# Optimization experiments

Measured on AMD Instinct MI355X. Metric: run time of the kernel, lower is better.

Reference implementation:

```python
import jax, jax.numpy as jnp
import numpy as np

EPS = 1e-5

def _neighbor_idx(H, W):
    # flat index of the 3x3 clamped neighborhood for each pixel, [H*W, 9]
    r = np.arange(H)[:, None, None]  # [H,1,1]
    c = np.arange(W)[None, :, None]  # [1,W,1]
    dr = np.repeat(np.array([-1, 0, 1]), 3)[None, None, :]  # [1,1,9]
    dc = np.tile(np.array([-1, 0, 1]), 3)[None, None, :]
    ri = np.clip(r + dr, 0, H - 1)
    ci = np.clip(c + dc, 0, W - 1)
    return jnp.asarray((ri * W + ci).reshape(H * W, 9))

def setup_inputs() -> dict:
    key = jax.random.key(0)
    ks = jax.random.split(key, 7)
    B, C, H, W = 16, 256, 80, 80
    s = 1.0 / np.sqrt(C)
    return {
        "x": jax.random.normal(ks[0], (B, C, H, W), jnp.float32),
        "Wq": jax.random.normal(ks[1], (C, C), jnp.float32) * s,
        "bq": jax.random.normal(ks[2], (C,), jnp.float32) * s,
        "Wk": jax.random.normal(ks[3], (C, C), jnp.float32) * s,
        "bk": jax.random.normal(ks[4], (C,), jnp.float32) * s,
        "Wv": jax.random.normal(ks[5], (C, C), jnp.float32) * s,
        "bv": jax.random.normal(ks[6], (C,), jnp.float32) * s,
    }

def reference(x, Wq, bq, Wk, bk, Wv, bv):
    B, C, H, W = x.shape
    N = H * W
    xf = x.reshape(B, C, N)
    # 1x1 convs as channel GEMMs
    q = jnp.einsum('oc,bcn->bno', Wq, xf) + bq          # [B,N,C]
    k = jnp.einsum('oc,bcn->bon', Wk, xf) + bk[:, None]  # [B,C,N]
    v = jnp.einsum('oc,bcn->bon', Wv, xf) + bv[:, None]  # [B,C,N]
    idx = _neighbor_idx(H, W)                            # [N,9]
    k_n = k[:, :, idx]                                   # [B,C,N,9]
    v_n = v[:, :, idx]                                   # [B,C,N,9]
    # raw attention scores (NOT softmaxed before AV, matching the source)
    scores = jnp.einsum('bnc,bcnq->bnq', q, k_n)         # [B,N,9]
    new_v = jnp.einsum('bnq,bcnq->bcn', scores, v_n).reshape(B, C, H, W)
    out9 = scores.reshape(B, H, W, 9)
    center = out9[..., 4]
    others_mean = (out9.sum(-1) - center) / 8.0
    output = jnp.stack([center, others_mean], axis=-1)   # [B,H,W,2]
    # residual + layer_norm over [H,W] (no affine), per (B,C)
    xr = x + new_v
    mu = xr.mean(axis=(-2, -1), keepdims=True)
    var = ((xr - mu) ** 2).mean(axis=(-2, -1), keepdims=True)
    x_out = (xr - mu) * jax.lax.rsqrt(var + EPS)
    return (output, x_out)
```

## Files before the change

kernel.cpp:

```cpp
#include <hip/hip_runtime.h>
#include <hip/hip_bf16.h>

using f32x4  = __attribute__((ext_vector_type(4))) float;
using short8 = __attribute__((ext_vector_type(8))) short;
using bf16   = __hip_bfloat16;

constexpr int BATCH = 16;
constexpr int CH    = 256;
constexpr int HH    = 80;
constexpr int WW    = 80;
constexpr int NPIX  = HH * WW;

__device__ __forceinline__ float b2f(unsigned short u) {
    union { unsigned int i; float f; } x;
    x.i = ((unsigned int)u) << 16;
    return x.f;
}

typedef __attribute__((address_space(3))) void  lds_void;
typedef __attribute__((address_space(1))) const void glb_void;
__device__ __forceinline__ void glds16(const void* g, void* l) {
    __builtin_amdgcn_global_load_lds((glb_void*)(unsigned long long)g,
                                     (lds_void*)(unsigned int)(unsigned long long)l,
                                     16, 0, 0);
}

__global__ __launch_bounds__(256) void convert_w(
    const float* __restrict__ Wq, const float* __restrict__ Wk,
    const float* __restrict__ Wv, bf16* __restrict__ Wb)
{
    const int elem = blockIdx.x * 256 + threadIdx.x;
    const int mat  = blockIdx.y;
    const float* src = (mat == 0) ? Wq : (mat == 1) ? Wk : Wv;
    Wb[(size_t)mat * CH * CH + elem] = __float2bfloat16(src[elem]);
}

__global__ __launch_bounds__(256) void transpose_cast(
    const float* __restrict__ x, bf16* __restrict__ xt, int b0)
{
    __shared__ float t[64][65];
    const int b  = b0 + blockIdx.z;
    const int n0 = blockIdx.x * 64;
    const int c0 = blockIdx.y * 64;
    const float* xb = x + (size_t)b * CH * NPIX;
    const int tid = threadIdx.x;

    {
        const int nl  = tid & 63;
        const int cl0 = tid >> 6;
        #pragma unroll
        for (int i = 0; i < 16; ++i) {
            const int cl = cl0 + i * 4;
            t[cl][nl] = xb[(size_t)(c0 + cl) * NPIX + n0 + nl];
        }
    }
    __syncthreads();
    {
        bf16* xtb = xt + (size_t)blockIdx.z * NPIX * CH;
        const int cp  = (tid & 15) * 4;
        const int nl0 = tid >> 4;
        #pragma unroll
        for (int i = 0; i < 4; ++i) {
            const int nl = nl0 + i * 16;
            ushort4 pk;
            #pragma unroll
            for (int j = 0; j < 4; ++j) {
                const bf16 h = __float2bfloat16(t[cp + j][nl]);
                ((unsigned short*)&pk)[j] = *(const unsigned short*)&h;
            }
            *(ushort4*)(xtb + (size_t)(n0 + nl) * CH + c0 + cp) = pk;
        }
    }
}

__global__ __launch_bounds__(256, 2) void qkv_mfma(
    const bf16* __restrict__ xt, const bf16* __restrict__ Wb,
    const float* __restrict__ bq, const float* __restrict__ bk,
    const float* __restrict__ bv,
    bf16* __restrict__ qt, bf16* __restrict__ kt, bf16* __restrict__ vt)
{
    const int bl = blockIdx.z;
    const int n0 = blockIdx.x * 128;
    const int o0 = blockIdx.y * 128;
    const bf16* A = xt + (size_t)bl * NPIX * CH;

    __shared__ char As[128 * 512];

    const int tid = threadIdx.x;
    const int wv  = tid >> 6, ln = tid & 63;
    const int wr  = wv >> 1,  wc = wv & 1;
    const int lm  = ln & 15,  lk = ln >> 4;

    #pragma unroll
    for (int t = 0; t < 16; ++t) {
        const int idx = t * 256 + tid;
        const int row = idx >> 5, pos = idx & 31;
        const int chk = pos ^ (row & 7);
        glds16(A + (size_t)(n0 + row) * CH + chk * 8, &As[idx * 16]);
    }

    const bf16* wl0 = Wb + (size_t)(o0 + wc * 64 + lm) * CH + lk * 8;
    const bf16* const wbase[3] = { wl0, wl0 + CH * CH, wl0 + 2 * CH * CH };

    bf16* const outs[3] = { qt + (size_t)bl * CH * NPIX,
                            kt + (size_t)bl * CH * NPIX,
                            vt + (size_t)bl * CH * NPIX };
    const float* const biases[3] = { bq, bk, bv };

    short8 fA[4], fB[4];
    #pragma unroll
    for (int j = 0; j < 4; ++j)
        fA[j] = *(const short8*)(wbase[0] + j * 16 * CH + 0);

    __syncthreads();

    #pragma unroll
    for (int m = 0; m < 3; ++m) {
        f32x4 acc[4][4];
        #pragma unroll
        for (int i = 0; i < 4; ++i)
            #pragma unroll
            for (int j = 0; j < 4; ++j)
                #pragma unroll
                for (int r = 0; r < 4; ++r) acc[i][j][r] = 0.f;

        #pragma unroll
        for (int t = 0; t < 8; ++t) {
            const int s = m * 8 + t;
            if (s < 23) {
                const int sn = s + 1;
                const int mn = sn >> 3, tn = sn & 7;
                #pragma unroll
                for (int j = 0; j < 4; ++j) {
                    const short8 v = *(const short8*)(wbase[mn] + j * 16 * CH + tn * 32);
                    if (t & 1) fA[j] = v; else fB[j] = v;
                }
            }

            short8 afr[4];
            #pragma unroll
            for (int i = 0; i < 4; ++i) {
                const int row = wr * 64 + i * 16 + lm;
                const int chunk = (t * 4 + lk) ^ (row & 7);
                afr[i] = *(const short8*)&As[row * 512 + chunk * 16];
            }
            #pragma unroll
            for (int i = 0; i < 4; ++i)
                #pragma unroll
                for (int j = 0; j < 4; ++j)
                    acc[i][j] = __builtin_amdgcn_mfma_f32_16x16x32_bf16(
                        afr[i], (t & 1) ? fB[j] : fA[j], acc[i][j], 0, 0, 0);
        }

        bf16* out = outs[m];
        const float* bias = biases[m];
        #pragma unroll
        for (int j = 0; j < 4; ++j) {
            const int o = o0 + wc * 64 + j * 16 + lm;
            const float bs = bias[o];
            #pragma unroll
            for (int i = 0; i < 4; ++i) {
                const int nb = n0 + wr * 64 + i * 16 + lk * 4;
                ushort4 pk;
                #pragma unroll
                for (int r = 0; r < 4; ++r) {
                    const bf16 h = __float2bfloat16(acc[i][j][r] + bs);
                    ((unsigned short*)&pk)[r] = *(const unsigned short*)&h;
                }
                *(ushort4*)(out + (size_t)o * NPIX + nb) = pk;
            }
        }
    }
}

__global__ __launch_bounds__(256) void scores_kernel(
    const bf16* __restrict__ qt, const bf16* __restrict__ kt,
    float* __restrict__ scores, float* __restrict__ out0, int b0)
{
    const int tid   = threadIdx.x;
    const int wave  = tid >> 6;
    const int lane  = tid & 63;
    const int ql    = lane & 7;
    const int chunk = lane >> 3;

    const int qi = blockIdx.x * 32 + wave * 8 + ql;
    const int bl = blockIdx.y;
    const int b  = b0 + bl;
    const int n0 = qi * 4;
    const int r  = qi / 20;
    const int p0 = n0 - r * WW;

    const unsigned short* qp = (const unsigned short*)(qt + (size_t)bl * NPIX * CH)
                               + (size_t)chunk * 32 * NPIX;
    const unsigned short* kp = (const unsigned short*)(kt + (size_t)bl * NPIX * CH)
                               + (size_t)chunk * 32 * NPIX;

    const int rbm = max(r - 1, 0) * WW;
    const int rb0 = r * WW;
    const int rbp = min(r + 1, HH - 1) * WW;
    const bool eL = (p0 == 0), eR = (p0 == 76);

    float acc[4][9];
    #pragma unroll
    for (int px = 0; px < 4; ++px)
        #pragma unroll
        for (int j = 0; j < 9; ++j) acc[px][j] = 0.f;

    #pragma unroll 4
    for (int c = 0; c < 32; ++c) {
        const size_t cb = (size_t)c * NPIX;
        const ushort4 qv = *(const ushort4*)(qp + cb + n0);
        const float qf0 = b2f(qv.x), qf1 = b2f(qv.y), qf2 = b2f(qv.z), qf3 = b2f(qv.w);

        #pragma unroll
        for (int dr = 0; dr < 3; ++dr) {
            const int rb = (dr == 0) ? rbm : (dr == 1) ? rb0 : rbp;
            const short8 kw = *(const short8*)(kp + cb + rb + p0 - 2);
            const float w3 = b2f((unsigned short)kw[1]);
            const float w4 = b2f((unsigned short)kw[2]);
            const float w5 = b2f((unsigned short)kw[3]);
            const float w6 = b2f((unsigned short)kw[4]);
            const float w7 = b2f((unsigned short)kw[5]);
            const float w8 = b2f((unsigned short)kw[6]);

            acc[0][dr*3+0] += qf0 * w3;
            acc[0][dr*3+1] += qf0 * w4;
            acc[0][dr*3+2] += qf0 * w5;
            acc[1][dr*3+0] += qf1 * w4;
            acc[1][dr*3+1] += qf1 * w5;
            acc[1][dr*3+2] += qf1 * w6;
            acc[2][dr*3+0] += qf2 * w5;
            acc[2][dr*3+1] += qf2 * w6;
            acc[2][dr*3+2] += qf2 * w7;
            acc[3][dr*3+0] += qf3 * w6;
            acc[3][dr*3+1] += qf3 * w7;
            acc[3][dr*3+2] += qf3 * w8;
            if (eL) acc[0][dr*3+0] += qf0 * (w4 - w3);
            if (eR) acc[3][dr*3+2] += qf3 * (w7 - w8);
        }
    }

    #pragma unroll
    for (int px = 0; px < 4; ++px)
        #pragma unroll
        for (int j = 0; j < 9; ++j) {
            float v = acc[px][j];
            v += __shfl_xor(v, 8,  64);
            v += __shfl_xor(v, 16, 64);
            v += __shfl_xor(v, 32, 64);
            acc[px][j] = v;
        }

    float* sp = scores + (size_t)bl * 9 * NPIX;
    if (chunk < 7) {
        float4 v = { acc[0][chunk], acc[1][chunk], acc[2][chunk], acc[3][chunk] };
        *(float4*)(sp + (size_t)chunk * NPIX + n0) = v;
    } else {
        float4 v7 = { acc[0][7], acc[1][7], acc[2][7], acc[3][7] };
        float4 v8 = { acc[0][8], acc[1][8], acc[2][8], acc[3][8] };
        *(float4*)(sp + (size_t)7 * NPIX + n0) = v7;
        *(float4*)(sp + (size_t)8 * NPIX + n0) = v8;
    }
    if (chunk == 0) {
        float ssum[4];
        #pragma unroll
        for (int px = 0; px < 4; ++px) {
            float s = 0.f;
            #pragma unroll
            for (int j = 0; j < 9; ++j) s += acc[px][j];
            ssum[px] = s;
        }
        float* op = out0 + ((size_t)b * NPIX + n0) * 2;
        float4 o0v = { acc[0][4], (ssum[0] - acc[0][4]) * 0.125f,
                       acc[1][4], (ssum[1] - acc[1][4]) * 0.125f };
        float4 o1v = { acc[2][4], (ssum[2] - acc[2][4]) * 0.125f,
                       acc[3][4], (ssum[3] - acc[3][4]) * 0.125f };
        *(float4*)(op)     = o0v;
        *(float4*)(op + 4) = o1v;
    }
}

__global__ __launch_bounds__(320) void newv_ln(
    const float* __restrict__ x, const bf16* __restrict__ vt,
    const float* __restrict__ scores, float* __restrict__ xout, int b0)
{
    __shared__ __align__(16) unsigned short lds_v[2][NPIX];
    __shared__ float rsum[5][2], rsq[5][2];

    const int cp2 = blockIdx.x;
    const int bl  = blockIdx.y;
    const int b   = b0 + bl;
    const int tid = threadIdx.x;

    const int4* vsrc = (const int4*)(vt + ((size_t)bl * CH + cp2 * 2) * NPIX);
    const float* xrow0 = x + ((size_t)b * CH + cp2 * 2) * NPIX;
    const float* xrow1 = xrow0 + NPIX;
    const float* sb    = scores + (size_t)bl * 9 * NPIX;

    #pragma unroll
    for (int i = 0; i < 5; ++i)
        ((int4*)lds_v)[tid + i * 320] = vsrc[tid + i * 320];
    __syncthreads();

    float val0[20], val1[20];
    float sum0 = 0.f, sq0 = 0.f, sum1 = 0.f, sq1 = 0.f;
    #pragma unroll
    for (int it = 0; it < 5; ++it) {
        const int p   = tid + it * 320;
        const int n0  = p * 4;
        const int r   = p / 20;
        const int c0  = (p % 20) * 4;

        const int rm = max(r - 1, 0) * WW;
        const int r0 = r * WW;
        const int rp = min(r + 1, HH - 1) * WW;

        float4 s[9];
        #pragma unroll
        for (int j = 0; j < 9; ++j)
            s[j] = *(const float4*)(sb + (size_t)j * NPIX + n0);

        const float4 xin0 = *(const float4*)(xrow0 + n0);
        const float4 xin1 = *(const float4*)(xrow1 + n0);

        const int cA = max(c0 - 1, 0);
        const int cF = min(c0 + 4, WW - 1);

        #pragma unroll
        for (int pl = 0; pl < 2; ++pl) {
            const unsigned short* lv = lds_v[pl];
            float vm[6], v0[6], vp[6];
            {
                const ushort4 a = *(const ushort4*)&lv[rm + c0];
                vm[1] = b2f(a.x); vm[2] = b2f(a.y); vm[3] = b2f(a.z); vm[4] = b2f(a.w);
                vm[0] = b2f(lv[rm + cA]); vm[5] = b2f(lv[rm + cF]);
            }
            {
                const ushort4 a = *(const ushort4*)&lv[r0 + c0];
                v0[1] = b2f(a.x); v0[2] = b2f(a.y); v0[3] = b2f(a.z); v0[4] = b2f(a.w);
                v0[0] = b2f(lv[r0 + cA]); v0[5] = b2f(lv[r0 + cF]);
            }
            {
                const ushort4 a = *(const ushort4*)&lv[rp + c0];
                vp[1] = b2f(a.x); vp[2] = b2f(a.y); vp[3] = b2f(a.z); vp[4] = b2f(a.w);
                vp[0] = b2f(lv[rp + cA]); vp[5] = b2f(lv[rp + cF]);
            }

            const float4 xin = pl ? xin1 : xin0;
            #pragma unroll
            for (int px = 0; px < 4; ++px) {
                float a;
                a  = ((const float*)&s[0])[px] * vm[px]
                   + ((const float*)&s[1])[px] * vm[px + 1]
                   + ((const float*)&s[2])[px] * vm[px + 2];
                a += ((const float*)&s[3])[px] * v0[px]
                   + ((const float*)&s[4])[px] * v0[px + 1]
                   + ((const float*)&s[5])[px] * v0[px + 2];
                a += ((const float*)&s[6])[px] * vp[px]
                   + ((const float*)&s[7])[px] * vp[px + 1]
                   + ((const float*)&s[8])[px] * vp[px + 2];
                const float vv = ((const float*)&xin)[px] + a;
                if (pl == 0) { val0[it * 4 + px] = vv; sum0 += vv; sq0 += vv * vv; }
                else         { val1[it * 4 + px] = vv; sum1 += vv; sq1 += vv * vv; }
            }
        }
    }

    #pragma unroll
    for (int off = 32; off >= 1; off >>= 1) {
        sum0 += __shfl_xor(sum0, off, 64);
        sq0  += __shfl_xor(sq0,  off, 64);
        sum1 += __shfl_xor(sum1, off, 64);
        sq1  += __shfl_xor(sq1,  off, 64);
    }
    const int wave = tid >> 6, lane = tid & 63;
    if (lane == 0) {
        rsum[wave][0] = sum0; rsq[wave][0] = sq0;
        rsum[wave][1] = sum1; rsq[wave][1] = sq1;
    }
    __syncthreads();
    sum0 = rsum[0][0] + rsum[1][0] + rsum[2][0] + rsum[3][0] + rsum[4][0];
    sq0  = rsq[0][0]  + rsq[1][0]  + rsq[2][0]  + rsq[3][0]  + rsq[4][0];
    sum1 = rsum[0][1] + rsum[1][1] + rsum[2][1] + rsum[3][1] + rsum[4][1];
    sq1  = rsq[0][1]  + rsq[1][1]  + rsq[2][1]  + rsq[3][1]  + rsq[4][1];

    const float mu0   = sum0 * (1.f / NPIX);
    const float var0  = sq0 * (1.f / NPIX) - mu0 * mu0;
    const float rstd0 = rsqrtf(var0 + 1e-5f);
    const float mu1   = sum1 * (1.f / NPIX);
    const float var1  = sq1 * (1.f / NPIX) - mu1 * mu1;
    const float rstd1 = rsqrtf(var1 + 1e-5f);

    float* orow0 = xout + ((size_t)b * CH + cp2 * 2) * NPIX;
    float* orow1 = orow0 + NPIX;
    #pragma unroll
    for (int it = 0; it < 5; ++it) {
        const int n0 = (tid + it * 320) * 4;
        float4 o0, o1;
        #pragma unroll
        for (int px = 0; px < 4; ++px) {
            ((float*)&o0)[px] = (val0[it * 4 + px] - mu0) * rstd0;
            ((float*)&o1)[px] = (val1[it * 4 + px] - mu1) * rstd1;
        }
        *(float4*)(orow0 + n0) = o0;
        *(float4*)(orow1 + n0) = o1;
    }
}

extern "C" void kernel_launch(void* const* d_in, const int* in_sizes, int n_in,
                              void* d_out, int out_size, void* d_ws, size_t ws_size,
                              hipStream_t stream)
{
    const float* x  = (const float*)d_in[0];
    const float* Wq = (const float*)d_in[1];
    const float* bq = (const float*)d_in[2];
    const float* Wk = (const float*)d_in[3];
    const float* bk = (const float*)d_in[4];
    const float* Wv = (const float*)d_in[5];
    const float* bv = (const float*)d_in[6];

    float* out0 = (float*)d_out;
    float* xout = out0 + (size_t)BATCH * NPIX * 2;

    char* ws = (char*)d_ws;
    bf16* Wb = (bf16*)ws;
    ws += (size_t)3 * CH * CH * sizeof(bf16);

    const size_t fBF = (size_t)NPIX * CH * sizeof(bf16);
    const size_t fSC = (size_t)NPIX * 9 * sizeof(float);
    const size_t perBatch = 4 * fBF + fSC;

    size_t avail = ws_size - ((size_t)3 * CH * CH * sizeof(bf16));
    int NB = (int)(avail / perBatch);
    if (NB < 1)  NB = 1;
    if (NB > BATCH) NB = BATCH;

    bf16*  xt  = (bf16*)ws;
    bf16*  qtb = (bf16*)(ws + (size_t)NB * fBF);
    bf16*  ktb = (bf16*)(ws + (size_t)NB * fBF * 2);
    bf16*  vtb = (bf16*)(ws + (size_t)NB * fBF * 3);
    float* sc  = (float*)(ws + (size_t)NB * fBF * 4);

    convert_w<<<dim3(CH * CH / 256, 3), 256, 0, stream>>>(Wq, Wk, Wv, Wb);

    for (int b0 = 0; b0 < BATCH; b0 += NB) {
        const int cnb = (BATCH - b0 < NB) ? (BATCH - b0) : NB;

        transpose_cast<<<dim3(NPIX / 64, CH / 64, cnb), 256, 0, stream>>>(x, xt, b0);

        qkv_mfma<<<dim3(NPIX / 128, CH / 128, cnb), 256, 0, stream>>>(
            xt, Wb, bq, bk, bv, qtb, ktb, vtb);

        scores_kernel<<<dim3(50, cnb), 256, 0, stream>>>(qtb, ktb, sc, out0, b0);

        newv_ln<<<dim3(CH / 2, cnb), 320, 0, stream>>>(x, vtb, sc, xout, b0);
    }
}
```

Measured before the change: 301.0 us.

## Stage QKV weight tiles through double-buffered LDS with register prefetch

In the QKV GEMM kernel, weight fragments were previously loaded straight from global memory into registers by each wave, with duplicate loads across waves. Now the block cooperatively loads each 128x32 weight slice two steps ahead into registers, writes it into a swizzled double-buffered LDS tile, and reads the MFMA B fragments from LDS. This removes redundant global weight traffic and hides load latency. In exchange it adds a barrier per k-step, extra LDS usage that may reduce occupancy, and hand-written waitcnt handling.

After: 330.3 us. +9.8%, slower.

```diff
diff --git a/kernel.cpp b/kernel.cpp
--- a/kernel.cpp
+++ b/kernel.cpp
@@ -85,6 +85,7 @@
     const bf16* A = xt + (size_t)bl * NPIX * CH;
 
     __shared__ char As[128 * 512];
+    __shared__ char Bs[2][128 * 64];
 
     const int tid = threadIdx.x;
     const int wv  = tid >> 6, ln = tid & 63;
@@ -99,21 +100,41 @@
         glds16(A + (size_t)(n0 + row) * CH + chk * 8, &As[idx * 16]);
     }
 
-    const bf16* wl0 = Wb + (size_t)(o0 + wc * 64 + lm) * CH + lk * 8;
-    const bf16* const wbase[3] = { wl0, wl0 + CH * CH, wl0 + 2 * CH * CH };
+    auto gload = [&](int s, int4* r) {
+        const int m  = s >> 3;
+        const int k0 = (s & 7) * 32;
+        const bf16* Wm = Wb + (size_t)m * CH * CH;
+        #pragma unroll
+        for (int it = 0; it < 2; ++it) {
+            const int idx = it * 256 + tid;
+            const int row = idx >> 2, pos = idx & 3;
+            const int chk = pos ^ ((row >> 1) & 3);
+            r[it] = *(const int4*)(Wm + (size_t)(o0 + row) * CH + k0 + chk * 8);
+        }
+    };
+    auto dswrite = [&](int buf, const int4* r) {
+        #pragma unroll
+        for (int it = 0; it < 2; ++it) {
+            const int idx = it * 256 + tid;
+            *(int4*)&Bs[buf][idx * 16] = r[it];
+        }
+    };
+
+    int4 R0[2], R1[2];
+    gload(0, R0);
+    gload(1, R1);
+    asm volatile("s_waitcnt vmcnt(2)" ::: "memory");
+    dswrite(0, R0);
+    asm volatile("s_waitcnt lgkmcnt(0)" ::: "memory");
+    __builtin_amdgcn_s_barrier();
+    __builtin_amdgcn_sched_barrier(0);
 
     bf16* const outs[3] = { qt + (size_t)bl * CH * NPIX,
                             kt + (size_t)bl * CH * NPIX,
                             vt + (size_t)bl * CH * NPIX };
     const float* const biases[3] = { bq, bk, bv };
 
-    short8 fA[4], fB[4];
-    #pragma unroll
-    for (int j = 0; j < 4; ++j)
-        fA[j] = *(const short8*)(wbase[0] + j * 16 * CH + 0);
-
-    __syncthreads();
-
+    int cur = 0;
     #pragma unroll
     for (int m = 0; m < 3; ++m) {
         f32x4 acc[4][4];
@@ -127,17 +148,15 @@
         #pragma unroll
         for (int t = 0; t < 8; ++t) {
             const int s = m * 8 + t;
-            if (s < 23) {
-                const int sn = s + 1;
-                const int mn = sn >> 3, tn = sn & 7;
-                #pragma unroll
-                for (int j = 0; j < 4; ++j) {
-                    const short8 v = *(const short8*)(wbase[mn] + j * 16 * CH + tn * 32);
-                    if (t & 1) fA[j] = v; else fB[j] = v;
-                }
-            }
-
-            short8 afr[4];
+
+            if (s + 2 <= 23) {
+                if ((s & 1) == 0) gload(s + 2, R0); else gload(s + 2, R1);
+            }
+            if (s + 1 <= 23) {
+                if ((s & 1) == 0) dswrite(cur ^ 1, R1); else dswrite(cur ^ 1, R0);
+            }
+
+            short8 afr[4], bfr[4];
             #pragma unroll
             for (int i = 0; i < 4; ++i) {
                 const int row = wr * 64 + i * 16 + lm;
@@ -145,11 +164,22 @@
                 afr[i] = *(const short8*)&As[row * 512 + chunk * 16];
             }
             #pragma unroll
+            for (int j = 0; j < 4; ++j) {
+                const int row = wc * 64 + j * 16 + lm;
+                const int chk = lk ^ ((row >> 1) & 3);
+                bfr[j] = *(const short8*)&Bs[cur][row * 64 + chk * 16];
+            }
+            #pragma unroll
             for (int i = 0; i < 4; ++i)
                 #pragma unroll
                 for (int j = 0; j < 4; ++j)
                     acc[i][j] = __builtin_amdgcn_mfma_f32_16x16x32_bf16(
-                        afr[i], (t & 1) ? fB[j] : fA[j], acc[i][j], 0, 0, 0);
+                        afr[i], bfr[j], acc[i][j], 0, 0, 0);
+
+            asm volatile("s_waitcnt lgkmcnt(0)" ::: "memory");
+            __builtin_amdgcn_s_barrier();
+            __builtin_amdgcn_sched_barrier(0);
+            cur ^= 1;
         }
 
         bf16* out = outs[m];
```
